# Optimization experiments

Hardware: AMD Instinct MI355X
Metric: run time of the kernel (lower is better)

## Reference

```python
import jax, jax.numpy as jnp
import numpy as np

B, H, W, D, C = 2, 16, 16, 16, 128
UNITS = 128
BN_EPS = 1e-3  # keras BatchNormalization default epsilon


def setup_inputs() -> dict:
    key = jax.random.key(0)
    ks = jax.random.split(key, 12)
    lim = np.sqrt(3.0 / C)  # VarianceScaling(1.0, fan_avg, uniform)
    inp = {
        "x": jax.random.normal(ks[0], (B, H, W, D, C), dtype=jnp.float32),
        "gamma": jnp.ones((C,), jnp.float32),
        "beta": jnp.zeros((C,), jnp.float32),
        "moving_mean": jax.random.normal(ks[1], (C,), jnp.float32) * 0.1,
        "moving_var": jnp.ones((C,), jnp.float32) + 0.1 * jax.random.uniform(ks[2], (C,)),
        "Wq": jax.random.uniform(ks[3], (C, UNITS), jnp.float32, -lim, lim),
        "bq": jnp.zeros((UNITS,), jnp.float32),
        "Wk": jax.random.uniform(ks[4], (C, UNITS), jnp.float32, -lim, lim),
        "bk": jnp.zeros((UNITS,), jnp.float32),
        "Wv": jax.random.uniform(ks[5], (C, UNITS), jnp.float32, -lim, lim),
        "bv": jnp.zeros((UNITS,), jnp.float32),
        # proj uses kernel_init(0.0) -> effectively ~0; use tiny scale to keep grads nonzero
        "Wp": jax.random.uniform(ks[6], (UNITS, UNITS), jnp.float32, -1e-5, 1e-5),
        "bp": jnp.zeros((UNITS,), jnp.float32),
    }
    return inp


def reference(x, gamma, beta, moving_mean, moving_var, Wq, bq, Wk, bk, Wv, bv, Wp, bp):
    # BatchNormalization (inference mode): per-channel affine normalization
    xn = (x - moving_mean) * jax.lax.rsqrt(moving_var + BN_EPS) * gamma + beta
    b, h, w, d, c = xn.shape
    n = h * w * d
    scale = jnp.asarray(UNITS, jnp.float32) ** -0.5
    q = (xn @ Wq + bq).reshape(b, n, UNITS)
    k = (xn @ Wk + bk).reshape(b, n, UNITS)
    v = (xn @ Wv + bv).reshape(b, n, UNITS)
    # full self-attention over flattened 3D spatial dims: [b, n, n] scores
    attn = jax.nn.softmax(jnp.einsum('bnc,bmc->bnm', q, k) * scale, axis=-1)
    proj = jnp.einsum('bnm,bmc->bnc', attn, v).reshape(b, h, w, d, UNITS)
    proj = proj @ Wp + bp
    return xn + proj
```

## Files before the change

kernel.cpp:

```cpp
#include <hip/hip_runtime.h>
#include <hip/hip_bf16.h>

using bh4     = __attribute__((ext_vector_type(4))) short;
using bh8     = __attribute__((ext_vector_type(8))) short;
using floatx4 = __attribute__((ext_vector_type(4))) float;

#define MFMA16 __builtin_amdgcn_mfma_f32_16x16x32_bf16

__device__ __forceinline__ float b2f(short s) {
    union { unsigned u; float f; } v; v.u = ((unsigned)(unsigned short)s) << 16; return v.f;
}
__device__ __forceinline__ short f2b(float f) {
    union { float f; unsigned u; } v; v.f = f;
    unsigned r = (v.u + 0x7fffu + ((v.u >> 16) & 1u)) >> 16;
    return (short)r;
}
__device__ __forceinline__ float ldf(const void* p, int i, bool f32) {
    return f32 ? ((const float*)p)[i] : b2f(((const short*)p)[i]);
}
__device__ __forceinline__ bool detect_f32(const void* gamma) {
    return ((*(const unsigned*)gamma) & 0xFFFFu) == 0u;
}

#define TLD 136
__global__ __launch_bounds__(256) void k_wT(
    const void* __restrict__ W0, const void* __restrict__ W1,
    const void* __restrict__ W2, const void* __restrict__ W3,
    short* __restrict__ WT, const void* __restrict__ gp)
{
    __shared__ __align__(16) short T[128 * TLD];
    const bool f32 = detect_f32(gp);
    const void* W = (blockIdx.x == 0) ? W0 : (blockIdx.x == 1) ? W1
                   : (blockIdx.x == 2) ? W2 : W3;
    const int tid = threadIdx.x;

    for (int it = 0; it < 8; ++it) {
        int f = (it * 256 + tid) * 8;
        int c = f >> 7, u = f & 127;
        short v[8];
        if (f32) {
            floatx4 a = *(const floatx4*)((const float*)W + f);
            floatx4 b = *(const floatx4*)((const float*)W + f + 4);
            #pragma unroll
            for (int j = 0; j < 4; ++j) { v[j] = f2b(a[j]); v[j + 4] = f2b(b[j]); }
        } else {
            bh8 a = *(const bh8*)((const short*)W + f);
            #pragma unroll
            for (int j = 0; j < 8; ++j) v[j] = a[j];
        }
        #pragma unroll
        for (int jj = 0; jj < 8; ++jj) {
            int j = (jj + tid) & 7;
            T[(u + j) * TLD + c] = v[j];
        }
    }
    __syncthreads();
    short* WTd = WT + blockIdx.x * 16384;
    for (int it = 0; it < 8; ++it) {
        int f = (it * 256 + tid) * 8;
        int u = f >> 7, c = f & 127;
        *(bh8*)(WTd + u * 128 + c) = *(const bh8*)(&T[u * TLD + c]);
    }
}

__global__ __launch_bounds__(256) void k_bn_qkv(
    const void* __restrict__ xp,
    const void* __restrict__ gp, const void* __restrict__ bep,
    const void* __restrict__ mmp, const void* __restrict__ mvp,
    const short* __restrict__ WT,
    const void* __restrict__ bqp, const void* __restrict__ bkp,
    const void* __restrict__ bvp,
    short* __restrict__ Qo, short* __restrict__ Ko, short* __restrict__ Vt)
{
    __shared__ float sS[128], sT[128];
    const bool f32 = detect_f32(gp);
    const int tid = threadIdx.x, wave = tid >> 6, lane = tid & 63;
    const int lq = lane >> 4, lr = lane & 15;
    const int row0 = blockIdx.x * 32;
    const int r2 = wave >> 1, uh = wave & 1;
    const int qrow = row0 + r2 * 16;

    if (tid < 128) {
        float ga = ldf(gp, tid, f32), be = ldf(bep, tid, f32);
        float mm = ldf(mmp, tid, f32), mv = ldf(mvp, tid, f32);
        float s = ga * rsqrtf(mv + 1e-3f);
        sS[tid] = s;
        sT[tid] = be - mm * s;
    }
    __syncthreads();

    bh8 a[4];
    #pragma unroll
    for (int ks = 0; ks < 4; ++ks) {
        int c0 = ks * 32 + lq * 8;
        floatx4 s0 = *(const floatx4*)(&sS[c0]), s1 = *(const floatx4*)(&sS[c0 + 4]);
        floatx4 t0 = *(const floatx4*)(&sT[c0]), t1 = *(const floatx4*)(&sT[c0 + 4]);
        bh8 af;
        if (f32) {
            const float* xr = (const float*)xp + (size_t)(qrow + lr) * 128 + c0;
            floatx4 x0 = *(const floatx4*)xr, x1 = *(const floatx4*)(xr + 4);
            #pragma unroll
            for (int j = 0; j < 4; ++j) {
                af[j]     = f2b(x0[j] * s0[j] + t0[j]);
                af[j + 4] = f2b(x1[j] * s1[j] + t1[j]);
            }
        } else {
            bh8 xv = *(const bh8*)((const short*)xp + (size_t)(qrow + lr) * 128 + c0);
            #pragma unroll
            for (int j = 0; j < 4; ++j) {
                af[j]     = f2b(b2f(xv[j]) * s0[j] + t0[j]);
                af[j + 4] = f2b(b2f(xv[j + 4]) * s1[j] + t1[j]);
            }
        }
        a[ks] = af;
    }

    #pragma unroll
    for (int g = 0; g < 3; ++g) {
        const short* WTg = WT + g * 16384;
        const void* bb = (g == 0) ? bqp : ((g == 1) ? bkp : bvp);
        floatx4 acc[4] = {};
        #pragma unroll
        for (int ks = 0; ks < 4; ++ks)
            #pragma unroll
            for (int t = 0; t < 4; ++t) {
                bh8 b = *(const bh8*)(WTg + (size_t)(uh * 64 + t * 16 + lr) * 128 + ks * 32 + lq * 8);
                acc[t] = MFMA16(a[ks], b, acc[t], 0, 0, 0);
            }
        #pragma unroll
        for (int t = 0; t < 4; ++t) {
            int u = uh * 64 + t * 16 + lr;
            float bias = ldf(bb, u, f32);
            #pragma unroll
            for (int r = 0; r < 4; ++r) {
                int grow = qrow + lq * 4 + r;
                short vb = f2b(acc[t][r] + bias);
                if (g == 0)      Qo[(size_t)grow * 128 + u] = vb;
                else if (g == 1) Ko[(size_t)grow * 128 + u] = vb;
                else {
                    int bsb = grow >> 12, n = grow & 4095;
                    Vt[(size_t)bsb * 128 * 4096 + (size_t)u * 4096 + n] = vb;
                }
            }
        }
    }
}

#define KLD 136
#define VLD 72
#define PLD 88

__global__ __launch_bounds__(256, 3) void k_attn(
    const short* __restrict__ Qg, const short* __restrict__ Kg,
    const short* __restrict__ Vt, short* __restrict__ Op,
    float* __restrict__ Lq)
{
    __shared__ __align__(16) short sK[64 * KLD];
    __shared__ __align__(16) short sV[128 * VLD];
    __shared__ __align__(16) short sP[4][16 * PLD];

    const int tid = threadIdx.x, wave = tid >> 6, lane = tid & 63;
    const int lq = lane >> 4, lr = lane & 15;
    const int qt = blockIdx.x >> 2, kq = blockIdx.x & 3;
    const int mq = qt * 64;
    const int bs = mq >> 12;
    const int key0q = kq * 1024;
    const short* Kb = Kg + (size_t)bs * 4096 * 128;
    const short* Vb = Vt + (size_t)bs * 128 * 4096;
    const int qrow = mq + wave * 16;

    bh8 aq[4];
    #pragma unroll
    for (int ks = 0; ks < 4; ++ks)
        aq[ks] = *(const bh8*)(Qg + (size_t)(qrow + lr) * 128 + ks * 32 + lq * 8);

    floatx4 accO[8] = {};
    float lsum[4] = {0.f, 0.f, 0.f, 0.f};
    const float c2 = 0.12751743f;
    const float m2 = 11.541560f;
    short* Pw = &sP[wave][0];

    for (int it = 0; it < 16; ++it) {
        const int key0 = key0q + it * 64;
        __syncthreads();
        #pragma unroll
        for (int rd = 0; rd < 4; ++rd) {
            int f = (rd * 256 + tid) * 8;
            int r = f >> 7, c = f & 127;
            *(bh8*)(&sK[r * KLD + c]) = *(const bh8*)(Kb + (size_t)(key0 + r) * 128 + c);
        }
        #pragma unroll
        for (int rd = 0; rd < 4; ++rd) {
            int f = (rd * 256 + tid) * 8;
            int r = f >> 6, c = f & 63;
            *(bh8*)(&sV[r * VLD + c]) = *(const bh8*)(Vb + (size_t)r * 4096 + key0 + c);
        }
        __syncthreads();

        floatx4 s[4];
        #pragma unroll
        for (int t = 0; t < 4; ++t) {
            floatx4 acc = {};
            #pragma unroll
            for (int ks = 0; ks < 4; ++ks) {
                bh8 b = *(const bh8*)(&sK[(t * 16 + lr) * KLD + ks * 32 + lq * 8]);
                acc = MFMA16(aq[ks], b, acc, 0, 0, 0);
            }
            s[t] = acc;
        }
        #pragma unroll
        for (int t = 0; t < 4; ++t)
            #pragma unroll
            for (int r = 0; r < 4; ++r)
                s[t][r] = exp2f(fmaf(s[t][r], c2, -m2));
        #pragma unroll
        for (int r = 0; r < 4; ++r)
            lsum[r] += (s[0][r] + s[1][r]) + (s[2][r] + s[3][r]);

        #pragma unroll
        for (int t = 0; t < 4; ++t)
            #pragma unroll
            for (int r = 0; r < 4; ++r)
                Pw[(lq * 4 + r) * PLD + t * 16 + lr] = f2b(s[t][r]);

        bh8 ap0 = *(const bh8*)(&Pw[lr * PLD + lq * 8]);
        bh8 ap1 = *(const bh8*)(&Pw[lr * PLD + 32 + lq * 8]);

        #pragma unroll
        for (int t = 0; t < 8; ++t) {
            bh8 b0 = *(const bh8*)(&sV[(t * 16 + lr) * VLD + lq * 8]);
            bh8 b1 = *(const bh8*)(&sV[(t * 16 + lr) * VLD + 32 + lq * 8]);
            accO[t] = MFMA16(ap0, b0, accO[t], 0, 0, 0);
            accO[t] = MFMA16(ap1, b1, accO[t], 0, 0, 0);
        }
    }

    #pragma unroll
    for (int r = 0; r < 4; ++r) {
        float v = lsum[r];
        v += __shfl_xor(v, 1, 16);
        v += __shfl_xor(v, 2, 16);
        v += __shfl_xor(v, 4, 16);
        v += __shfl_xor(v, 8, 16);
        lsum[r] = v;
    }
    if (lr == 0) {
        #pragma unroll
        for (int r = 0; r < 4; ++r)
            Lq[(size_t)kq * 8192 + qrow + lq * 4 + r] = lsum[r];
    }
    short* Ob = Op + (size_t)kq * 8192 * 128;
    #pragma unroll
    for (int t = 0; t < 8; ++t)
        #pragma unroll
        for (int r = 0; r < 4; ++r)
            Ob[(size_t)(qrow + lq * 4 + r) * 128 + t * 16 + lr] = f2b(accO[t][r]);
}

__global__ __launch_bounds__(256) void k_comb(
    const short* __restrict__ Op, const float* __restrict__ Lq,
    short* __restrict__ O)
{
    const int idx = (blockIdx.x * 256 + threadIdx.x) * 8;
    const int row = idx >> 7;
    float L = Lq[row] + Lq[8192 + row] + Lq[16384 + row] + Lq[24576 + row];
    float invL = 1.0f / L;
    float sum[8] = {};
    #pragma unroll
    for (int w = 0; w < 4; ++w) {
        bh8 p = *(const bh8*)(Op + (size_t)w * 8192 * 128 + idx);
        #pragma unroll
        for (int j = 0; j < 8; ++j) sum[j] += b2f(p[j]);
    }
    bh8 o;
    #pragma unroll
    for (int j = 0; j < 8; ++j) o[j] = f2b(sum[j] * invL);
    *(bh8*)(O + idx) = o;
}

__global__ __launch_bounds__(256) void k_proj(
    const short* __restrict__ O, const short* __restrict__ WpT,
    const void* __restrict__ bpp, const void* __restrict__ xp,
    const void* __restrict__ gp, const void* __restrict__ bep,
    const void* __restrict__ mmp, const void* __restrict__ mvp,
    void* __restrict__ outp)
{
    __shared__ float sS[128], sT[128];
    const bool f32 = detect_f32(gp);
    const int tid = threadIdx.x, wave = tid >> 6, lane = tid & 63;
    const int lq = lane >> 4, lr = lane & 15;
    const int uh = blockIdx.x & 1;
    const int row0 = (blockIdx.x >> 1) * 64;
    const int arow = row0 + wave * 16;

    if (tid < 128) {
        float ga = ldf(gp, tid, f32), be = ldf(bep, tid, f32);
        float mm = ldf(mmp, tid, f32), mv = ldf(mvp, tid, f32);
        float s = ga * rsqrtf(mv + 1e-3f);
        sS[tid] = s;
        sT[tid] = be - mm * s;
    }
    __syncthreads();

    bh8 a[4];
    #pragma unroll
    for (int ks = 0; ks < 4; ++ks)
        a[ks] = *(const bh8*)(O + (size_t)(arow + lr) * 128 + ks * 32 + lq * 8);

    floatx4 acc[4] = {};
    #pragma unroll
    for (int ks = 0; ks < 4; ++ks)
        #pragma unroll
        for (int t = 0; t < 4; ++t) {
            bh8 b = *(const bh8*)(WpT + (size_t)(uh * 64 + t * 16 + lr) * 128 + ks * 32 + lq * 8);
            acc[t] = MFMA16(a[ks], b, acc[t], 0, 0, 0);
        }

    #pragma unroll
    for (int t = 0; t < 4; ++t) {
        int u = uh * 64 + t * 16 + lr;
        float bias = ldf(bpp, u, f32);
        float su = sS[u], tu = sT[u];
        #pragma unroll
        for (int r = 0; r < 4; ++r) {
            int grow = arow + lq * 4 + r;
            float xnv = ldf(xp, grow * 128 + u, f32) * su + tu;
            float v = acc[t][r] + bias + xnv;
            size_t idx = (size_t)grow * 128 + u;
            if (f32) ((float*)outp)[idx] = v;
            else     ((short*)outp)[idx] = f2b(v);
        }
    }
}

extern "C" void kernel_launch(void* const* d_in, const int* in_sizes, int n_in,
                              void* d_out, int out_size, void* d_ws, size_t ws_size,
                              hipStream_t stream)
{
    const void* x     = d_in[0];
    const void* gamma = d_in[1];
    const void* beta  = d_in[2];
    const void* mmean = d_in[3];
    const void* mvar  = d_in[4];
    const void* Wq    = d_in[5];
    const void* bq    = d_in[6];
    const void* Wk    = d_in[7];
    const void* bk    = d_in[8];
    const void* Wv    = d_in[9];
    const void* bv    = d_in[10];
    const void* Wp    = d_in[11];
    const void* bp    = d_in[12];

    char* ws = (char*)d_ws;
    const size_t MB = 1024u * 1024u;
    short* WT    = (short*)(ws + 0 * MB);
    short* Q     = (short*)(ws + 1 * MB);
    short* K     = (short*)(ws + 3 * MB);
    short* Vt    = (short*)(ws + 5 * MB);
    short* Opart = (short*)(ws + 7 * MB);
    short* O     = (short*)(ws + 15 * MB);
    float* Lsum  = (float*)(ws + 17 * MB);

    k_wT<<<4, 256, 0, stream>>>(Wq, Wk, Wv, Wp, WT, gamma);
    k_bn_qkv<<<256, 256, 0, stream>>>(x, gamma, beta, mmean, mvar,
                                      WT, bq, bk, bv, Q, K, Vt);
    k_attn<<<512, 256, 0, stream>>>(Q, K, Vt, Opart, Lsum);
    k_comb<<<512, 256, 0, stream>>>(Opart, Lsum, O);
    k_proj<<<256, 256, 0, stream>>>(O, WT + 3 * 16384, bp, x,
                                    gamma, beta, mmean, mvar, d_out);
}
```

Before: 150.5 us.

## Drop weight-transpose and combine kernels, fuse split-K combine into projection

Removes the separate weight-transpose kernel: the QKV and projection GEMMs now gather B fragments straight from the original row-major weights, converting each element to bf16 on the fly. The QKV kernel is split so each block computes only one of Q, K or V (768 blocks instead of 256). The split-K combine kernel is folded into the projection kernel, which sums the four partial outputs and normalizes by the summed denominators while loading its A operand. This saves two launches and the intermediate O round trip. In exchange, the weight loads become strided scalar gathers with redundant conversions across blocks, and x is re-read three times for BN.

```diff
diff --git a/kernel.cpp b/kernel.cpp
--- a/kernel.cpp
+++ b/kernel.cpp
@@ -22,63 +22,31 @@
     return ((*(const unsigned*)gamma) & 0xFFFFu) == 0u;
 }
 
-#define TLD 136
-__global__ __launch_bounds__(256) void k_wT(
-    const void* __restrict__ W0, const void* __restrict__ W1,
-    const void* __restrict__ W2, const void* __restrict__ W3,
-    short* __restrict__ WT, const void* __restrict__ gp)
-{
-    __shared__ __align__(16) short T[128 * TLD];
-    const bool f32 = detect_f32(gp);
-    const void* W = (blockIdx.x == 0) ? W0 : (blockIdx.x == 1) ? W1
-                   : (blockIdx.x == 2) ? W2 : W3;
-    const int tid = threadIdx.x;
-
-    for (int it = 0; it < 8; ++it) {
-        int f = (it * 256 + tid) * 8;
-        int c = f >> 7, u = f & 127;
-        short v[8];
-        if (f32) {
-            floatx4 a = *(const floatx4*)((const float*)W + f);
-            floatx4 b = *(const floatx4*)((const float*)W + f + 4);
-            #pragma unroll
-            for (int j = 0; j < 4; ++j) { v[j] = f2b(a[j]); v[j + 4] = f2b(b[j]); }
-        } else {
-            bh8 a = *(const bh8*)((const short*)W + f);
-            #pragma unroll
-            for (int j = 0; j < 8; ++j) v[j] = a[j];
-        }
-        #pragma unroll
-        for (int jj = 0; jj < 8; ++jj) {
-            int j = (jj + tid) & 7;
-            T[(u + j) * TLD + c] = v[j];
-        }
-    }
-    __syncthreads();
-    short* WTd = WT + blockIdx.x * 16384;
-    for (int it = 0; it < 8; ++it) {
-        int f = (it * 256 + tid) * 8;
-        int u = f >> 7, c = f & 127;
-        *(bh8*)(WTd + u * 128 + c) = *(const bh8*)(&T[u * TLD + c]);
-    }
+__device__ __forceinline__ bh8 wfrag(const void* W, int ks, int lq, int u, bool f32) {
+    bh8 b;
+    #pragma unroll
+    for (int j = 0; j < 8; ++j)
+        b[j] = f2b(ldf(W, (ks * 32 + lq * 8 + j) * 128 + u, f32));
+    return b;
 }
 
 __global__ __launch_bounds__(256) void k_bn_qkv(
     const void* __restrict__ xp,
     const void* __restrict__ gp, const void* __restrict__ bep,
     const void* __restrict__ mmp, const void* __restrict__ mvp,
-    const short* __restrict__ WT,
-    const void* __restrict__ bqp, const void* __restrict__ bkp,
-    const void* __restrict__ bvp,
+    const void* __restrict__ Wqp, const void* __restrict__ bqp,
+    const void* __restrict__ Wkp, const void* __restrict__ bkp,
+    const void* __restrict__ Wvp, const void* __restrict__ bvp,
     short* __restrict__ Qo, short* __restrict__ Ko, short* __restrict__ Vt)
 {
     __shared__ float sS[128], sT[128];
     const bool f32 = detect_f32(gp);
     const int tid = threadIdx.x, wave = tid >> 6, lane = tid & 63;
     const int lq = lane >> 4, lr = lane & 15;
-    const int row0 = blockIdx.x * 32;
-    const int r2 = wave >> 1, uh = wave & 1;
-    const int qrow = row0 + r2 * 16;
+    const int g = blockIdx.x >> 8;
+    const int tile = blockIdx.x & 255;
+    const int qrow = tile * 32 + (wave >> 1) * 16;
+    const int u0 = (wave & 1) * 64;
 
     if (tid < 128) {
         float ga = ldf(gp, tid, f32), be = ldf(bep, tid, f32);
@@ -115,32 +83,31 @@
         a[ks] = af;
     }
 
-    #pragma unroll
-    for (int g = 0; g < 3; ++g) {
-        const short* WTg = WT + g * 16384;
-        const void* bb = (g == 0) ? bqp : ((g == 1) ? bkp : bvp);
-        floatx4 acc[4] = {};
-        #pragma unroll
-        for (int ks = 0; ks < 4; ++ks)
-            #pragma unroll
-            for (int t = 0; t < 4; ++t) {
-                bh8 b = *(const bh8*)(WTg + (size_t)(uh * 64 + t * 16 + lr) * 128 + ks * 32 + lq * 8);
-                acc[t] = MFMA16(a[ks], b, acc[t], 0, 0, 0);
-            }
+    const void* W  = (g == 0) ? Wqp : ((g == 1) ? Wkp : Wvp);
+    const void* bb = (g == 0) ? bqp : ((g == 1) ? bkp : bvp);
+
+    floatx4 acc[4] = {};
+    #pragma unroll
+    for (int ks = 0; ks < 4; ++ks)
         #pragma unroll
         for (int t = 0; t < 4; ++t) {
-            int u = uh * 64 + t * 16 + lr;
-            float bias = ldf(bb, u, f32);
-            #pragma unroll
-            for (int r = 0; r < 4; ++r) {
-                int grow = qrow + lq * 4 + r;
-                short vb = f2b(acc[t][r] + bias);
-                if (g == 0)      Qo[(size_t)grow * 128 + u] = vb;
-                else if (g == 1) Ko[(size_t)grow * 128 + u] = vb;
-                else {
-                    int bsb = grow >> 12, n = grow & 4095;
-                    Vt[(size_t)bsb * 128 * 4096 + (size_t)u * 4096 + n] = vb;
-                }
+            bh8 b = wfrag(W, ks, lq, u0 + t * 16 + lr, f32);
+            acc[t] = MFMA16(a[ks], b, acc[t], 0, 0, 0);
+        }
+
+    #pragma unroll
+    for (int t = 0; t < 4; ++t) {
+        int u = u0 + t * 16 + lr;
+        float bias = ldf(bb, u, f32);
+        #pragma unroll
+        for (int r = 0; r < 4; ++r) {
+            int grow = qrow + lq * 4 + r;
+            short vb = f2b(acc[t][r] + bias);
+            if (g == 0)      Qo[(size_t)grow * 128 + u] = vb;
+            else if (g == 1) Ko[(size_t)grow * 128 + u] = vb;
+            else {
+                int bsb = grow >> 12, n = grow & 4095;
+                Vt[(size_t)bsb * 128 * 4096 + (size_t)u * 4096 + n] = vb;
             }
         }
     }
@@ -257,30 +224,10 @@
             Ob[(size_t)(qrow + lq * 4 + r) * 128 + t * 16 + lr] = f2b(accO[t][r]);
 }
 
-__global__ __launch_bounds__(256) void k_comb(
+__global__ __launch_bounds__(256) void k_proj(
     const short* __restrict__ Op, const float* __restrict__ Lq,
-    short* __restrict__ O)
-{
-    const int idx = (blockIdx.x * 256 + threadIdx.x) * 8;
-    const int row = idx >> 7;
-    float L = Lq[row] + Lq[8192 + row] + Lq[16384 + row] + Lq[24576 + row];
-    float invL = 1.0f / L;
-    float sum[8] = {};
-    #pragma unroll
-    for (int w = 0; w < 4; ++w) {
-        bh8 p = *(const bh8*)(Op + (size_t)w * 8192 * 128 + idx);
-        #pragma unroll
-        for (int j = 0; j < 8; ++j) sum[j] += b2f(p[j]);
-    }
-    bh8 o;
-    #pragma unroll
-    for (int j = 0; j < 8; ++j) o[j] = f2b(sum[j] * invL);
-    *(bh8*)(O + idx) = o;
-}
-
-__global__ __launch_bounds__(256) void k_proj(
-    const short* __restrict__ O, const short* __restrict__ WpT,
-    const void* __restrict__ bpp, const void* __restrict__ xp,
+    const void* __restrict__ Wpp, const void* __restrict__ bpp,
+    const void* __restrict__ xp,
     const void* __restrict__ gp, const void* __restrict__ bep,
     const void* __restrict__ mmp, const void* __restrict__ mvp,
     void* __restrict__ outp)
@@ -290,8 +237,9 @@
     const int tid = threadIdx.x, wave = tid >> 6, lane = tid & 63;
     const int lq = lane >> 4, lr = lane & 15;
     const int uh = blockIdx.x & 1;
-    const int row0 = (blockIdx.x >> 1) * 64;
-    const int arow = row0 + wave * 16;
+    const int tile = blockIdx.x >> 1;
+    const int arow = tile * 32 + (wave >> 1) * 16;
+    const int uo0 = uh * 64 + (wave & 1) * 32;
 
     if (tid < 128) {
         float ga = ldf(gp, tid, f32), be = ldf(bep, tid, f32);
@@ -302,23 +250,38 @@
     }
     __syncthreads();
 
+    const int myrow = arow + lr;
+    float L = Lq[myrow] + Lq[8192 + myrow] + Lq[16384 + myrow] + Lq[24576 + myrow];
+    const float invL = 1.0f / L;
+
     bh8 a[4];
     #pragma unroll
+    for (int ks = 0; ks < 4; ++ks) {
+        float sum[8] = {};
+        #pragma unroll
+        for (int w = 0; w < 4; ++w) {
+            bh8 p = *(const bh8*)(Op + (size_t)w * 8192 * 128 + (size_t)myrow * 128 + ks * 32 + lq * 8);
+            #pragma unroll
+            for (int j = 0; j < 8; ++j) sum[j] += b2f(p[j]);
+        }
+        bh8 af;
+        #pragma unroll
+        for (int j = 0; j < 8; ++j) af[j] = f2b(sum[j] * invL);
+        a[ks] = af;
+    }
+
+    floatx4 acc[2] = {};
+    #pragma unroll
     for (int ks = 0; ks < 4; ++ks)
-        a[ks] = *(const bh8*)(O + (size_t)(arow + lr) * 128 + ks * 32 + lq * 8);
-
-    floatx4 acc[4] = {};
-    #pragma unroll
-    for (int ks = 0; ks < 4; ++ks)
-        #pragma unroll
-        for (int t = 0; t < 4; ++t) {
-            bh8 b = *(const bh8*)(WpT + (size_t)(uh * 64 + t * 16 + lr) * 128 + ks * 32 + lq * 8);
+        #pragma unroll
+        for (int t = 0; t < 2; ++t) {
+            bh8 b = wfrag(Wpp, ks, lq, uo0 + t * 16 + lr, f32);
             acc[t] = MFMA16(a[ks], b, acc[t], 0, 0, 0);
         }
 
     #pragma unroll
-    for (int t = 0; t < 4; ++t) {
-        int u = uh * 64 + t * 16 + lr;
+    for (int t = 0; t < 2; ++t) {
+        int u = uo0 + t * 16 + lr;
         float bias = ldf(bpp, u, f32);
         float su = sS[u], tu = sT[u];
         #pragma unroll
@@ -353,19 +316,15 @@
 
     char* ws = (char*)d_ws;
     const size_t MB = 1024u * 1024u;
-    short* WT    = (short*)(ws + 0 * MB);
-    short* Q     = (short*)(ws + 1 * MB);
-    short* K     = (short*)(ws + 3 * MB);
-    short* Vt    = (short*)(ws + 5 * MB);
-    short* Opart = (short*)(ws + 7 * MB);
-    short* O     = (short*)(ws + 15 * MB);
-    float* Lsum  = (float*)(ws + 17 * MB);
-
-    k_wT<<<4, 256, 0, stream>>>(Wq, Wk, Wv, Wp, WT, gamma);
-    k_bn_qkv<<<256, 256, 0, stream>>>(x, gamma, beta, mmean, mvar,
-                                      WT, bq, bk, bv, Q, K, Vt);
+    short* Q     = (short*)(ws + 0 * MB);
+    short* K     = (short*)(ws + 2 * MB);
+    short* Vt    = (short*)(ws + 4 * MB);
+    short* Opart = (short*)(ws + 6 * MB);
+    float* Lsum  = (float*)(ws + 14 * MB);
+
+    k_bn_qkv<<<768, 256, 0, stream>>>(x, gamma, beta, mmean, mvar,
+                                      Wq, bq, Wk, bk, Wv, bv, Q, K, Vt);
     k_attn<<<512, 256, 0, stream>>>(Q, K, Vt, Opart, Lsum);
-    k_comb<<<512, 256, 0, stream>>>(Opart, Lsum, O);
-    k_proj<<<256, 256, 0, stream>>>(O, WT + 3 * 16384, bp, x,
+    k_proj<<<512, 256, 0, stream>>>(Opart, Lsum, Wp, bp, x,
                                     gamma, beta, mmean, mvar, d_out);
 }
```

Measured after the change: 145.8 us. -3.2%, faster.
